# Kernel optimization log

Measured on AMD Instinct MI355X. Metric: run time of the kernel, lower is better.

Reference implementation:

```python
import jax, jax.numpy as jnp
import numpy as np

NUM_GRAPHS = 512
NODES_PER_GRAPH = 200  # == N_rois
EDGES_PER_GRAPH = 3200  # avg degree 16
N_ROIS = 200
HIDDEN = 64
OUT = 2


def setup_inputs() -> dict:
    key = jax.random.key(0)
    ks = jax.random.split(key, 7)
    N = NUM_GRAPHS * NODES_PER_GRAPH
    E = NUM_GRAPHS * EDGES_PER_GRAPH
    x = jax.random.normal(ks[0], (N, N_ROIS), dtype=jnp.float32)
    # edges sampled within each graph's node block
    base = jnp.repeat(jnp.arange(NUM_GRAPHS, dtype=jnp.int64) * NODES_PER_GRAPH, EDGES_PER_GRAPH)
    local = jax.random.randint(ks[1], (2, E), 0, NODES_PER_GRAPH, dtype=jnp.int64)
    edge_index = local + base[None, :]
    batch = jnp.arange(N, dtype=jnp.int64) // NODES_PER_GRAPH
    conv_w = jax.random.normal(ks[2], (N_ROIS, HIDDEN), dtype=jnp.float32) * 0.1
    conv_b = jax.random.normal(ks[3], (HIDDEN,), dtype=jnp.float32) * 0.1
    lin_w = jax.random.normal(ks[4], (HIDDEN, OUT), dtype=jnp.float32) * 0.1
    lin_b = jax.random.normal(ks[5], (OUT,), dtype=jnp.float32) * 0.1
    return {"x": x, "edge_index": edge_index, "batch": batch,
            "conv_w": conv_w, "conv_b": conv_b, "lin_w": lin_w, "lin_b": lin_b}


def reference(x, edge_index, batch, conv_w, conv_b, lin_w, lin_b):
    N = x.shape[0]
    # GCNConv: linear transform first (N_rois -> hidden), then normalized aggregation
    h = x @ conv_w  # [N, H]
    loops = jnp.arange(N, dtype=edge_index.dtype)
    src = jnp.concatenate([edge_index[0], loops])  # add self-loops (PyG default)
    dst = jnp.concatenate([edge_index[1], loops])
    deg = jax.ops.segment_sum(jnp.ones_like(dst, dtype=h.dtype), dst, num_segments=N)
    dinv = jnp.where(deg > 0, jax.lax.rsqrt(deg), jnp.zeros_like(deg))
    norm = dinv[src] * dinv[dst]  # D^-1/2 (A+I) D^-1/2 edge weights
    agg = jax.ops.segment_sum(h[src] * norm[:, None], dst, num_segments=N) + conv_b
    hr = jax.nn.relu(agg)
    x_pool = jax.ops.segment_max(hr, batch, num_segments=NUM_GRAPHS)  # [G, H]
    out = x_pool @ lin_w + lin_b  # [G, OUT]
    return out, x_pool
```

## Files before the change

kernel.cpp:

```cpp
#include <hip/hip_runtime.h>

#define NUM_GRAPHS 512
#define NPG 200
#define EPG 3200
#define NROIS 200
#define HID 64
#define OUTC 2
#define APITCH 232
#define HPITCH 232
#define XPITCH 40
#define WIMG_ELEMS (7 * 4 * 2 * 64 * 8)
#define WS_NEEDED ((size_t)WIMG_ELEMS * 2)

typedef short v8s __attribute__((ext_vector_type(8)));
typedef float v4f __attribute__((ext_vector_type(4)));

__device__ __forceinline__ unsigned bf16_rne(float f) {
  unsigned u = __float_as_uint(f);
  return (u + 0x7fffu + ((u >> 16) & 1u)) >> 16;
}

__global__ void prep_wimg(const float* __restrict__ cw, unsigned short* __restrict__ wimg) {
  int idx = blockIdx.x * 256 + threadIdx.x;
  if (idx >= WIMG_ELEMS) return;
  int i    = idx & 7;
  int lane = (idx >> 3) & 63;
  int hl   = (idx >> 9) & 1;
  int nt   = (idx >> 10) & 3;
  int kt   = idx >> 12;
  int k  = kt * 32 + (lane >> 4) * 8 + i;
  int ch = nt * 16 + (lane & 15);
  float f = (k < NROIS) ? cw[k * HID + ch] : 0.f;
  unsigned hi = bf16_rne(f);
  float lo = f - __uint_as_float(hi << 16);
  wimg[idx] = hl ? (unsigned short)(__float_as_uint(lo) >> 16) : (unsigned short)hi;
}

struct __align__(16) SmemU {
  unsigned char adj[208 * APITCH];
  union {
    unsigned short xb[2][NPG * XPITCH];
    unsigned short hpTl[HID * HPITCH];
  } u;
  float dinv[NPG];
  int pool[HID];
};

__device__ __forceinline__ void xload(float4* xf, const float* __restrict__ x,
                                      int base, int c0, int tid) {
  #pragma unroll
  for (int r = 0; r < 4; ++r) {
    int idx = tid + r * 512;
    int node = idx >> 3, f4 = idx & 7;
    int col = c0 + f4 * 4;
    if (idx < 1600 && col + 4 <= NROIS)
      xf[r] = *(const float4*)(x + (size_t)(base + node) * NROIS + col);
    else
      xf[r] = make_float4(0.f, 0.f, 0.f, 0.f);
  }
}

__device__ __forceinline__ void xwrite(SmemU& s, int buf, const float4* xf, int tid) {
  #pragma unroll
  for (int r = 0; r < 4; ++r) {
    int idx = tid + r * 512;
    if (idx < 1600) {
      int node = idx >> 3, f4 = idx & 7;
      unsigned b0 = bf16_rne(xf[r].x), b1 = bf16_rne(xf[r].y);
      unsigned b2 = bf16_rne(xf[r].z), b3 = bf16_rne(xf[r].w);
      uint2 p = {b0 | (b1 << 16), b2 | (b3 << 16)};
      *(uint2*)&s.u.xb[buf][node * XPITCH + f4 * 4] = p;
    }
  }
}

__global__ __launch_bounds__(512, 4)
void gcn_fused4(const float* __restrict__ x,
                const int* __restrict__ ei,
                const unsigned short* __restrict__ wimg,
                const float* __restrict__ cb,
                const float* __restrict__ lw,
                const float* __restrict__ lb,
                float* __restrict__ out,
                int Etot) {
  __shared__ SmemU s;
  const int g = blockIdx.x;
  const int tid = threadIdx.x;
  const int base = g * NPG;
  const int ebase = g * EPG;
  const int lane = tid & 63;
  const int w = __builtin_amdgcn_readfirstlane(tid >> 6);
  const int ml = tid & 15;
  const int q  = (tid >> 4) & 3;

  float4 xf[4];
  xload(xf, x, base, 0, tid);
  int esrc[7], edst[7];
  #pragma unroll
  for (int r = 0; r < 7; ++r) {
    int e = tid + r * 512;
    esrc[r] = -1; edst[r] = 0;
    if (e < EPG) {
      esrc[r] = ei[ebase + e] - base;
      edst[r] = ei[Etot + ebase + e] - base;
    }
  }
  {
    uint4* z = (uint4*)s.adj;
    const uint4 z4 = {0u, 0u, 0u, 0u};
    #pragma unroll
    for (int i = 0; i < 6; ++i) {
      int idx = tid + i * 512;
      if (idx < (208 * APITCH) / 16) z[idx] = z4;
    }
    if (tid < HID) s.pool[tid] = 0;
  }
  __syncthreads();

  {
    unsigned* adjW = (unsigned*)s.adj;
    #pragma unroll
    for (int r = 0; r < 7; ++r) {
      if (esrc[r] >= 0) {
        int idx = edst[r] * APITCH + esrc[r];
        atomicAdd(&adjW[idx >> 2], 1u << ((idx & 3) * 8));
      }
    }
    if (tid < NPG) {
      int idx = tid * APITCH + tid;
      atomicAdd(&adjW[idx >> 2], 1u << ((idx & 3) * 8));
    }
  }
  xwrite(s, 0, xf, tid);
  __syncthreads();

  {
    int row = tid >> 1, half = tid & 1;
    if (row < NPG) {
      const unsigned* ap = (const unsigned*)s.adj + row * (APITCH / 4) + half * 29;
      unsigned ssum = 0;
      #pragma unroll 4
      for (int j = 0; j < 29; ++j)
        ssum += (ap[j] * 0x01010101u) >> 24;
      ssum += __shfl_xor((int)ssum, 1);
      if (half == 0) s.dinv[row] = rsqrtf((float)ssum);
    }
  }

  int mts[2];
  mts[0] = w;
  mts[1] = (w < 5) ? 8 + w : -1;

  v4f acc[2][4];
  #pragma unroll
  for (int a = 0; a < 2; ++a)
    #pragma unroll
    for (int b = 0; b < 4; ++b)
      acc[a][b] = (v4f){0.f, 0.f, 0.f, 0.f};

  for (int kt = 0; kt < 7; ++kt) {
    float4 xfn[4];
    if (kt < 6) xload(xfn, x, base, (kt + 1) * 32, tid);

    v8s whi[4], wlo[4];
    #pragma unroll
    for (int nt = 0; nt < 4; ++nt) {
      const unsigned short* pw = wimg + (size_t)(((kt * 4 + nt) * 2) * 64 + lane) * 8;
      whi[nt] = *(const v8s*)pw;
      wlo[nt] = *(const v8s*)(pw + 64 * 8);
    }
    #pragma unroll
    for (int mi = 0; mi < 2; ++mi) {
      if (mts[mi] >= 0) {
        const int node = mts[mi] * 16 + ml;
        const int nrd = (node < NPG) ? node : 0;
        const v8s xh = *(const v8s*)&s.u.xb[kt & 1][nrd * XPITCH + q * 8];
        #pragma unroll
        for (int nt = 0; nt < 4; ++nt) {
          acc[mi][nt] = __builtin_amdgcn_mfma_f32_16x16x32_bf16(wlo[nt], xh, acc[mi][nt], 0, 0, 0);
          acc[mi][nt] = __builtin_amdgcn_mfma_f32_16x16x32_bf16(whi[nt], xh, acc[mi][nt], 0, 0, 0);
        }
      }
    }
    if (kt < 6) xwrite(s, (kt + 1) & 1, xfn, tid);
    __syncthreads();
  }

  {
    int ch = tid >> 3, grp = tid & 7;
    *(uint2*)&s.u.hpTl[ch * HPITCH + 200 + grp * 4] = (uint2){0u, 0u};
  }
  #pragma unroll
  for (int mi = 0; mi < 2; ++mi) {
    if (mts[mi] >= 0) {
      const int node = mts[mi] * 16 + ml;
      if (node < NPG) {
        const float dv = s.dinv[node];
        #pragma unroll
        for (int nt = 0; nt < 4; ++nt) {
          #pragma unroll
          for (int r = 0; r < 4; ++r) {
            const int ch = nt * 16 + q * 4 + r;
            s.u.hpTl[ch * HPITCH + node] = (unsigned short)bf16_rne(dv * acc[mi][nt][r]);
          }
        }
      }
    }
  }
  __syncthreads();

  {
    v4f acc2[2][4];
    #pragma unroll
    for (int a = 0; a < 2; ++a)
      #pragma unroll
      for (int b = 0; b < 4; ++b)
        acc2[a][b] = (v4f){0.f, 0.f, 0.f, 0.f};

    for (int kt = 0; kt < 7; ++kt) {
      const int k0 = kt * 32 + q * 8;

      v8s bf[4];
      #pragma unroll
      for (int nt = 0; nt < 4; ++nt)
        bf[nt] = *(const v8s*)&s.u.hpTl[(nt * 16 + ml) * HPITCH + k0];

      #pragma unroll
      for (int mi = 0; mi < 2; ++mi) {
        if (mts[mi] >= 0) {
          const int row = mts[mi] * 16 + ml;
          const uint2 dd = *(const uint2*)&s.adj[row * APITCH + k0];
          v8s af;
          #pragma unroll
          for (int i = 0; i < 4; ++i) {
            af[i]     = (short)(__float_as_uint((float)((dd.x >> (8 * i)) & 0xffu)) >> 16);
            af[i + 4] = (short)(__float_as_uint((float)((dd.y >> (8 * i)) & 0xffu)) >> 16);
          }
          #pragma unroll
          for (int nt = 0; nt < 4; ++nt)
            acc2[mi][nt] = __builtin_amdgcn_mfma_f32_16x16x32_bf16(af, bf[nt], acc2[mi][nt], 0, 0, 0);
        }
      }
    }

    float cbv[4];
    #pragma unroll
    for (int nt = 0; nt < 4; ++nt) cbv[nt] = cb[nt * 16 + ml];
    float mx[4] = {0.f, 0.f, 0.f, 0.f};
    #pragma unroll
    for (int mi = 0; mi < 2; ++mi) {
      if (mts[mi] >= 0) {
        #pragma unroll
        for (int r = 0; r < 4; ++r) {
          const int row = mts[mi] * 16 + q * 4 + r;
          if (row < NPG) {
            const float dv = s.dinv[row];
            #pragma unroll
            for (int nt = 0; nt < 4; ++nt) {
              float v = fmaxf(fmaf(dv, acc2[mi][nt][r], cbv[nt]), 0.f);
              mx[nt] = fmaxf(mx[nt], v);
            }
          }
        }
      }
    }
    #pragma unroll
    for (int nt = 0; nt < 4; ++nt) {
      mx[nt] = fmaxf(mx[nt], __shfl_xor(mx[nt], 16));
      mx[nt] = fmaxf(mx[nt], __shfl_xor(mx[nt], 32));
    }
    if (q == 0 && (lane >> 5) == 0) {
      #pragma unroll
      for (int nt = 0; nt < 4; ++nt)
        atomicMax(&s.pool[nt * 16 + ml], __float_as_int(mx[nt]));
    }
  }
  __syncthreads();

  if (tid < HID) {
    const float xp = __int_as_float(s.pool[tid]);
    out[NUM_GRAPHS * OUTC + g * HID + tid] = xp;
    float p0 = xp * lw[tid * 2 + 0];
    float p1 = xp * lw[tid * 2 + 1];
    #pragma unroll
    for (int off = 32; off > 0; off >>= 1) {
      p0 += __shfl_down(p0, off);
      p1 += __shfl_down(p1, off);
    }
    if (tid == 0) {
      out[g * OUTC + 0] = p0 + lb[0];
      out[g * OUTC + 1] = p1 + lb[1];
    }
  }
}

struct __align__(16) SmemF {
  unsigned char adj[208 * APITCH];
  unsigned short hpT[HID * HPITCH];
  float dinv[NPG];
  int cnt[NPG];
  int pool[HID];
};

__global__ __launch_bounds__(512, 4)
void gcn_fused_fb(const float* __restrict__ x,
                  const int* __restrict__ ei,
                  const float* __restrict__ cw,
                  const float* __restrict__ cb,
                  const float* __restrict__ lw,
                  const float* __restrict__ lb,
                  float* __restrict__ out,
                  int Etot) {
  __shared__ SmemF s;
  const int g = blockIdx.x;
  const int tid = threadIdx.x;
  const int base = g * NPG;
  const int ebase = g * EPG;
  const int lane = tid & 63;
  const int w = __builtin_amdgcn_readfirstlane(tid >> 6);
  const int ml = tid & 15;
  const int q  = (tid >> 4) & 3;

  {
    uint4* z = (uint4*)&s;
    const uint4 z4 = {0u, 0u, 0u, 0u};
    #pragma unroll
    for (int i = 0; i < 10; ++i) {
      int idx = tid + i * 512;
      if (idx < (208 * APITCH + HID * HPITCH * 2) / 16) z[idx] = z4;
    }
    if (tid < NPG) s.cnt[tid] = 0;
    if (tid < HID) s.pool[tid] = 0;
  }
  __syncthreads();

  int esrc[7], edst[7];
  #pragma unroll
  for (int r = 0; r < 7; ++r) {
    int e = tid + r * 512;
    esrc[r] = -1; edst[r] = 0;
    if (e < EPG) {
      esrc[r] = ei[ebase + e] - base;
      edst[r] = ei[Etot + ebase + e] - base;
      atomicAdd(&s.cnt[edst[r]], 1);
    }
  }
  __syncthreads();

  if (tid < NPG) s.dinv[tid] = rsqrtf((float)(s.cnt[tid] + 1));

  {
    unsigned* adjW = (unsigned*)s.adj;
    #pragma unroll
    for (int r = 0; r < 7; ++r) {
      if (esrc[r] >= 0) {
        int idx = edst[r] * APITCH + esrc[r];
        atomicAdd(&adjW[idx >> 2], 1u << ((idx & 3) * 8));
      }
    }
    if (tid < NPG) {
      int idx = tid * APITCH + tid;
      atomicAdd(&adjW[idx >> 2], 1u << ((idx & 3) * 8));
    }
  }
  __syncthreads();

  {
    int mts[2];
    mts[0] = w;
    mts[1] = (w < 5) ? 8 + w : -1;
    v4f acc[2][4];
    #pragma unroll
    for (int a = 0; a < 2; ++a)
      #pragma unroll
      for (int b = 0; b < 4; ++b)
        acc[a][b] = (v4f){0.f, 0.f, 0.f, 0.f};

    for (int kt = 0; kt < 7; ++kt) {
      const int k0 = kt * 32 + q * 8;
      const bool kok = (k0 < NROIS);
      v8s bhi[4], blo[4];
      #pragma unroll
      for (int nt = 0; nt < 4; ++nt) {
        #pragma unroll
        for (int i = 0; i < 8; ++i) {
          float f = kok ? cw[(k0 + i) * HID + nt * 16 + ml] : 0.f;
          unsigned hb = bf16_rne(f);
          float lo = f - __uint_as_float(hb << 16);
          bhi[nt][i] = (short)hb;
          blo[nt][i] = (short)(__float_as_uint(lo) >> 16);
        }
      }
      #pragma unroll
      for (int mi = 0; mi < 2; ++mi) {
        if (mts[mi] >= 0) {
          const int row = mts[mi] * 16 + ml;
          v8s ahi, alo;
          if (kok && row < NPG) {
            const float* px = x + (size_t)(base + row) * NROIS + k0;
            const float4 f0 = *(const float4*)px;
            const float4 f1 = *(const float4*)(px + 4);
            const float ff[8] = {f0.x, f0.y, f0.z, f0.w, f1.x, f1.y, f1.z, f1.w};
            #pragma unroll
            for (int i = 0; i < 8; ++i) {
              unsigned u = __float_as_uint(ff[i]);
              unsigned hb = u >> 16;
              float lo = ff[i] - __uint_as_float(hb << 16);
              ahi[i] = (short)hb;
              alo[i] = (short)(__float_as_uint(lo) >> 16);
            }
          } else {
            #pragma unroll
            for (int i = 0; i < 8; ++i) { ahi[i] = 0; alo[i] = 0; }
          }
          #pragma unroll
          for (int nt = 0; nt < 4; ++nt) {
            acc[mi][nt] = __builtin_amdgcn_mfma_f32_16x16x32_bf16(ahi, blo[nt], acc[mi][nt], 0, 0, 0);
            acc[mi][nt] = __builtin_amdgcn_mfma_f32_16x16x32_bf16(alo, bhi[nt], acc[mi][nt], 0, 0, 0);
            acc[mi][nt] = __builtin_amdgcn_mfma_f32_16x16x32_bf16(ahi, bhi[nt], acc[mi][nt], 0, 0, 0);
          }
        }
      }
    }
    #pragma unroll
    for (int mi = 0; mi < 2; ++mi) {
      if (mts[mi] >= 0) {
        #pragma unroll
        for (int r = 0; r < 4; ++r) {
          const int row = mts[mi] * 16 + q * 4 + r;
          if (row < NPG) {
            const float dv = s.dinv[row];
            #pragma unroll
            for (int nt = 0; nt < 4; ++nt)
              s.hpT[(nt * 16 + ml) * HPITCH + row] =
                  (unsigned short)bf16_rne(dv * acc[mi][nt][r]);
          }
        }
      }
    }
  }
  __syncthreads();

  {
    int mts[2];
    mts[0] = w;
    mts[1] = (w < 5) ? 8 + w : -1;
    v4f acc2[2][4];
    #pragma unroll
    for (int a = 0; a < 2; ++a)
      #pragma unroll
      for (int b = 0; b < 4; ++b)
        acc2[a][b] = (v4f){0.f, 0.f, 0.f, 0.f};

    for (int kt = 0; kt < 7; ++kt) {
      const int k0 = kt * 32 + q * 8;
      v8s bf[4];
      #pragma unroll
      for (int nt = 0; nt < 4; ++nt)
        bf[nt] = *(const v8s*)&s.hpT[(nt * 16 + ml) * HPITCH + k0];
      #pragma unroll
      for (int mi = 0; mi < 2; ++mi) {
        if (mts[mi] >= 0) {
          const int row = mts[mi] * 16 + ml;
          const uint2 dd = *(const uint2*)&s.adj[row * APITCH + k0];
          v8s af;
          #pragma unroll
          for (int i = 0; i < 4; ++i) {
            af[i]     = (short)(__float_as_uint((float)((dd.x >> (8 * i)) & 0xffu)) >> 16);
            af[i + 4] = (short)(__float_as_uint((float)((dd.y >> (8 * i)) & 0xffu)) >> 16);
          }
          #pragma unroll
          for (int nt = 0; nt < 4; ++nt)
            acc2[mi][nt] = __builtin_amdgcn_mfma_f32_16x16x32_bf16(af, bf[nt], acc2[mi][nt], 0, 0, 0);
        }
      }
    }

    float cbv[4];
    #pragma unroll
    for (int nt = 0; nt < 4; ++nt) cbv[nt] = cb[nt * 16 + ml];
    float mx[4] = {0.f, 0.f, 0.f, 0.f};
    #pragma unroll
    for (int mi = 0; mi < 2; ++mi) {
      if (mts[mi] >= 0) {
        #pragma unroll
        for (int r = 0; r < 4; ++r) {
          const int row = mts[mi] * 16 + q * 4 + r;
          if (row < NPG) {
            const float dv = s.dinv[row];
            #pragma unroll
            for (int nt = 0; nt < 4; ++nt) {
              float v = fmaxf(fmaf(dv, acc2[mi][nt][r], cbv[nt]), 0.f);
              mx[nt] = fmaxf(mx[nt], v);
            }
          }
        }
      }
    }
    #pragma unroll
    for (int nt = 0; nt < 4; ++nt) {
      mx[nt] = fmaxf(mx[nt], __shfl_xor(mx[nt], 16));
      mx[nt] = fmaxf(mx[nt], __shfl_xor(mx[nt], 32));
    }
    if (q == 0 && (lane >> 5) == 0) {
      #pragma unroll
      for (int nt = 0; nt < 4; ++nt)
        atomicMax(&s.pool[nt * 16 + ml], __float_as_int(mx[nt]));
    }
  }
  __syncthreads();

  if (tid < HID) {
    const float xp = __int_as_float(s.pool[tid]);
    out[NUM_GRAPHS * OUTC + g * HID + tid] = xp;
    float p0 = xp * lw[tid * 2 + 0];
    float p1 = xp * lw[tid * 2 + 1];
    #pragma unroll
    for (int off = 32; off > 0; off >>= 1) {
      p0 += __shfl_down(p0, off);
      p1 += __shfl_down(p1, off);
    }
    if (tid == 0) {
      out[g * OUTC + 0] = p0 + lb[0];
      out[g * OUTC + 1] = p1 + lb[1];
    }
  }
}

extern "C" void kernel_launch(void* const* d_in, const int* in_sizes, int n_in,
                              void* d_out, int out_size, void* d_ws, size_t ws_size,
                              hipStream_t stream) {
  const float* x  = (const float*)d_in[0];
  const int*   ei = (const int*)d_in[1];
  const float* cw = (const float*)d_in[3];
  const float* cb = (const float*)d_in[4];
  const float* lw = (const float*)d_in[5];
  const float* lb = (const float*)d_in[6];
  const int Etot = in_sizes[1] / 2;

  if (ws_size >= WS_NEEDED) {
    unsigned short* wimg = (unsigned short*)d_ws;
    prep_wimg<<<(WIMG_ELEMS + 255) / 256, 256, 0, stream>>>(cw, wimg);
    gcn_fused4<<<NUM_GRAPHS, 512, 0, stream>>>(x, ei, wimg, cb, lw, lb,
                                               (float*)d_out, Etot);
  } else {
    gcn_fused_fb<<<NUM_GRAPHS, 512, 0, stream>>>(x, ei, cw, cb, lw, lb,
                                                 (float*)d_out, Etot);
  }
}
```

Baseline: 150.1 us.

## Load x directly into MFMA registers and count degrees with atomics

Drops the LDS staging of x: each lane now fetches the rows it needs straight from global memory into registers, converts them to bf16, and prefetches the next k-tile. This removes the per-iteration __syncthreads in the first GEMM loop. Node degree is now accumulated with an atomic counter per destination while the adjacency is built, replacing the row-sum scan over the adjacency matrix. The cost is an extra LDS atomic per edge, loss of the union so LDS use grows, and global loads that are less coalesced.

```diff
diff --git a/kernel.cpp b/kernel.cpp
--- a/kernel.cpp
+++ b/kernel.cpp
@@ -8,7 +8,6 @@
 #define OUTC 2
 #define APITCH 232
 #define HPITCH 232
-#define XPITCH 40
 #define WIMG_ELEMS (7 * 4 * 2 * 64 * 8)
 #define WS_NEEDED ((size_t)WIMG_ELEMS * 2)
 
@@ -36,46 +35,45 @@
   wimg[idx] = hl ? (unsigned short)(__float_as_uint(lo) >> 16) : (unsigned short)hi;
 }
 
-struct __align__(16) SmemU {
+struct __align__(16) Smem2 {
   unsigned char adj[208 * APITCH];
-  union {
-    unsigned short xb[2][NPG * XPITCH];
-    unsigned short hpTl[HID * HPITCH];
-  } u;
+  unsigned short hpTl[HID * HPITCH];
+  int cnt[NPG];
   float dinv[NPG];
   int pool[HID];
 };
 
-__device__ __forceinline__ void xload(float4* xf, const float* __restrict__ x,
-                                      int base, int c0, int tid) {
+__device__ __forceinline__ v8s tobf16(const float4& a, const float4& b) {
+  v8s r;
+  r[0] = (short)bf16_rne(a.x); r[1] = (short)bf16_rne(a.y);
+  r[2] = (short)bf16_rne(a.z); r[3] = (short)bf16_rne(a.w);
+  r[4] = (short)bf16_rne(b.x); r[5] = (short)bf16_rne(b.y);
+  r[6] = (short)bf16_rne(b.z); r[7] = (short)bf16_rne(b.w);
+  return r;
+}
+
+__device__ __forceinline__ void xfetch(const float* __restrict__ x, int base,
+                                       int kt, int q, const int* mts, const int* nrow,
+                                       float4 xa[2][2]) {
+  const int k0 = kt * 32 + q * 8;
+  const bool ok = (k0 + 8 <= NROIS);
   #pragma unroll
-  for (int r = 0; r < 4; ++r) {
-    int idx = tid + r * 512;
-    int node = idx >> 3, f4 = idx & 7;
-    int col = c0 + f4 * 4;
-    if (idx < 1600 && col + 4 <= NROIS)
-      xf[r] = *(const float4*)(x + (size_t)(base + node) * NROIS + col);
-    else
-      xf[r] = make_float4(0.f, 0.f, 0.f, 0.f);
-  }
-}
-
-__device__ __forceinline__ void xwrite(SmemU& s, int buf, const float4* xf, int tid) {
-  #pragma unroll
-  for (int r = 0; r < 4; ++r) {
-    int idx = tid + r * 512;
-    if (idx < 1600) {
-      int node = idx >> 3, f4 = idx & 7;
-      unsigned b0 = bf16_rne(xf[r].x), b1 = bf16_rne(xf[r].y);
-      unsigned b2 = bf16_rne(xf[r].z), b3 = bf16_rne(xf[r].w);
-      uint2 p = {b0 | (b1 << 16), b2 | (b3 << 16)};
-      *(uint2*)&s.u.xb[buf][node * XPITCH + f4 * 4] = p;
+  for (int mi = 0; mi < 2; ++mi) {
+    if (mts[mi] >= 0) {
+      if (ok) {
+        const float* px = x + (size_t)(base + nrow[mi]) * NROIS + k0;
+        xa[mi][0] = *(const float4*)px;
+        xa[mi][1] = *(const float4*)(px + 4);
+      } else {
+        xa[mi][0] = make_float4(0.f, 0.f, 0.f, 0.f);
+        xa[mi][1] = make_float4(0.f, 0.f, 0.f, 0.f);
+      }
     }
   }
 }
 
 __global__ __launch_bounds__(512, 4)
-void gcn_fused4(const float* __restrict__ x,
+void gcn_fused5(const float* __restrict__ x,
                 const int* __restrict__ ei,
                 const unsigned short* __restrict__ wimg,
                 const float* __restrict__ cb,
@@ -83,7 +81,7 @@
                 const float* __restrict__ lb,
                 float* __restrict__ out,
                 int Etot) {
-  __shared__ SmemU s;
+  __shared__ Smem2 s;
   const int g = blockIdx.x;
   const int tid = threadIdx.x;
   const int base = g * NPG;
@@ -93,8 +91,16 @@
   const int ml = tid & 15;
   const int q  = (tid >> 4) & 3;
 
-  float4 xf[4];
-  xload(xf, x, base, 0, tid);
+  int mts[2];
+  mts[0] = w;
+  mts[1] = (w < 5) ? 8 + w : -1;
+  int nrow[2];
+  #pragma unroll
+  for (int mi = 0; mi < 2; ++mi) {
+    int node = mts[mi] * 16 + ml;
+    nrow[mi] = (node < NPG) ? node : 0;
+  }
+
   int esrc[7], edst[7];
   #pragma unroll
   for (int r = 0; r < 7; ++r) {
@@ -105,6 +111,8 @@
       edst[r] = ei[Etot + ebase + e] - base;
     }
   }
+  float4 xa[2][2];
+  xfetch(x, base, 0, q, mts, nrow, xa);
   {
     uint4* z = (uint4*)s.adj;
     const uint4 z4 = {0u, 0u, 0u, 0u};
@@ -113,6 +121,7 @@
       int idx = tid + i * 512;
       if (idx < (208 * APITCH) / 16) z[idx] = z4;
     }
+    if (tid < NPG) s.cnt[tid] = 0;
     if (tid < HID) s.pool[tid] = 0;
   }
   __syncthreads();
@@ -124,6 +133,7 @@
       if (esrc[r] >= 0) {
         int idx = edst[r] * APITCH + esrc[r];
         atomicAdd(&adjW[idx >> 2], 1u << ((idx & 3) * 8));
+        atomicAdd(&s.cnt[edst[r]], 1);
       }
     }
     if (tid < NPG) {
@@ -131,25 +141,6 @@
       atomicAdd(&adjW[idx >> 2], 1u << ((idx & 3) * 8));
     }
   }
-  xwrite(s, 0, xf, tid);
-  __syncthreads();
-
-  {
-    int row = tid >> 1, half = tid & 1;
-    if (row < NPG) {
-      const unsigned* ap = (const unsigned*)s.adj + row * (APITCH / 4) + half * 29;
-      unsigned ssum = 0;
-      #pragma unroll 4
-      for (int j = 0; j < 29; ++j)
-        ssum += (ap[j] * 0x01010101u) >> 24;
-      ssum += __shfl_xor((int)ssum, 1);
-      if (half == 0) s.dinv[row] = rsqrtf((float)ssum);
-    }
-  }
-
-  int mts[2];
-  mts[0] = w;
-  mts[1] = (w < 5) ? 8 + w : -1;
 
   v4f acc[2][4];
   #pragma unroll
@@ -159,8 +150,11 @@
       acc[a][b] = (v4f){0.f, 0.f, 0.f, 0.f};
 
   for (int kt = 0; kt < 7; ++kt) {
-    float4 xfn[4];
-    if (kt < 6) xload(xfn, x, base, (kt + 1) * 32, tid);
+    v8s xh2[2];
+    #pragma unroll
+    for (int mi = 0; mi < 2; ++mi)
+      if (mts[mi] >= 0) xh2[mi] = tobf16(xa[mi][0], xa[mi][1]);
+    if (kt < 6) xfetch(x, base, kt + 1, q, mts, nrow, xa);
 
     v8s whi[4], wlo[4];
     #pragma unroll
@@ -172,36 +166,33 @@
     #pragma unroll
     for (int mi = 0; mi < 2; ++mi) {
       if (mts[mi] >= 0) {
-        const int node = mts[mi] * 16 + ml;
-        const int nrd = (node < NPG) ? node : 0;
-        const v8s xh = *(const v8s*)&s.u.xb[kt & 1][nrd * XPITCH + q * 8];
         #pragma unroll
         for (int nt = 0; nt < 4; ++nt) {
-          acc[mi][nt] = __builtin_amdgcn_mfma_f32_16x16x32_bf16(wlo[nt], xh, acc[mi][nt], 0, 0, 0);
-          acc[mi][nt] = __builtin_amdgcn_mfma_f32_16x16x32_bf16(whi[nt], xh, acc[mi][nt], 0, 0, 0);
-        }
-      }
-    }
-    if (kt < 6) xwrite(s, (kt + 1) & 1, xfn, tid);
-    __syncthreads();
-  }
-
+          acc[mi][nt] = __builtin_amdgcn_mfma_f32_16x16x32_bf16(wlo[nt], xh2[mi], acc[mi][nt], 0, 0, 0);
+          acc[mi][nt] = __builtin_amdgcn_mfma_f32_16x16x32_bf16(whi[nt], xh2[mi], acc[mi][nt], 0, 0, 0);
+        }
+      }
+    }
+  }
+  __syncthreads();
+
+  if (tid < NPG) s.dinv[tid] = rsqrtf((float)(s.cnt[tid] + 1));
   {
     int ch = tid >> 3, grp = tid & 7;
-    *(uint2*)&s.u.hpTl[ch * HPITCH + 200 + grp * 4] = (uint2){0u, 0u};
+    *(uint2*)&s.hpTl[ch * HPITCH + 200 + grp * 4] = (uint2){0u, 0u};
   }
   #pragma unroll
   for (int mi = 0; mi < 2; ++mi) {
     if (mts[mi] >= 0) {
       const int node = mts[mi] * 16 + ml;
       if (node < NPG) {
-        const float dv = s.dinv[node];
+        const float dv = rsqrtf((float)(s.cnt[node] + 1));
         #pragma unroll
         for (int nt = 0; nt < 4; ++nt) {
           #pragma unroll
           for (int r = 0; r < 4; ++r) {
             const int ch = nt * 16 + q * 4 + r;
-            s.u.hpTl[ch * HPITCH + node] = (unsigned short)bf16_rne(dv * acc[mi][nt][r]);
+            s.hpTl[ch * HPITCH + node] = (unsigned short)bf16_rne(dv * acc[mi][nt][r]);
           }
         }
       }
@@ -223,7 +214,7 @@
       v8s bf[4];
       #pragma unroll
       for (int nt = 0; nt < 4; ++nt)
-        bf[nt] = *(const v8s*)&s.u.hpTl[(nt * 16 + ml) * HPITCH + k0];
+        bf[nt] = *(const v8s*)&s.hpTl[(nt * 16 + ml) * HPITCH + k0];
 
       #pragma unroll
       for (int mi = 0; mi < 2; ++mi) {
@@ -541,7 +532,7 @@
   if (ws_size >= WS_NEEDED) {
     unsigned short* wimg = (unsigned short*)d_ws;
     prep_wimg<<<(WIMG_ELEMS + 255) / 256, 256, 0, stream>>>(cw, wimg);
-    gcn_fused4<<<NUM_GRAPHS, 512, 0, stream>>>(x, ei, wimg, cb, lw, lb,
+    gcn_fused5<<<NUM_GRAPHS, 512, 0, stream>>>(x, ei, wimg, cb, lw, lb,
                                                (float*)d_out, Etot);
   } else {
     gcn_fused_fb<<<NUM_GRAPHS, 512, 0, stream>>>(x, ei, cw, cb, lw, lb,
```

New measurement: 151.1 us. Within noise of the previous version (+0.7%).
